# Kernel optimization log

Measured on AMD Instinct MI355X. Metric: run time of the kernel, lower is better.

## Reference

```python
import jax, jax.numpy as jnp
import numpy as np

MESSAGE_SIZE = 128
MESSAGE_PASSES = 3
N_BONDS = 7      # Single, Double, Triple, Quadruple, Aromatic, Pi, Universal
N_LAYERS = 8     # 8 bias-free Linear layers, ReLU after the first 7
N_TYPES = 6      # top-4 ranked atoms + atom 0, plus catchall slot (index 5)
ATOM_VALS = [6.0, 7.0, 8.0, 9.0, 16.0, 17.0, 1.0]
TOP_ATOMS = [6.0, 7.0, 8.0, 9.0, 0.0]


def setup_inputs() -> dict:
    key = jax.random.key(0)
    ks = jax.random.split(key, 8)
    B, N, F, D = 128, 128, 75, MESSAGE_SIZE
    g = jax.random.uniform(ks[0], (B, N_BONDS, N, N), dtype=jnp.float32)
    h = jax.random.normal(ks[1], (B, N, F), dtype=jnp.float32)
    # channel 0 carries the atomic number used for GRU routing
    atom_ids = jax.random.randint(ks[2], (B, N), 0, len(ATOM_VALS))
    h = h.at[:, :, 0].set(jnp.asarray(ATOM_VALS, jnp.float32)[atom_ids])
    s = 1.0 / np.sqrt(D)
    msg_W = jax.random.normal(ks[3], (N_BONDS, N_LAYERS, D, D), jnp.float32) * s
    gru_Wih = jax.random.normal(ks[4], (2, N_TYPES, 3 * D, D), jnp.float32) * s  # [regular/universal, type, 3H, H]
    gru_Whh = jax.random.normal(ks[5], (2, N_TYPES, 3 * D, D), jnp.float32) * s
    gru_bih = jax.random.normal(ks[6], (2, N_TYPES, 3 * D), jnp.float32) * s
    gru_bhh = jax.random.normal(ks[7], (2, N_TYPES, 3 * D), jnp.float32) * s
    return dict(g=g, h=h, msg_W=msg_W, gru_Wih=gru_Wih, gru_Whh=gru_Whh,
                gru_bih=gru_bih, gru_bhh=gru_bhh)


def _gru_grouped(x, hx, tid, Wih, Whh, bih, bhh):
    """torch.nn.GRUCell(input=x, hx=hx) with per-node parameter group tid in [0,T).
    Wih/Whh: [T, 3H, H], bih/bhh: [T, 3H]."""
    gx = jnp.einsum('nd,tgd->ntg', x, Wih)   # [n, T, 3H]
    gh = jnp.einsum('nd,tgd->ntg', hx, Whh)
    gx = jnp.take_along_axis(gx, tid[:, None, None], axis=1)[:, 0] + bih[tid]
    gh = jnp.take_along_axis(gh, tid[:, None, None], axis=1)[:, 0] + bhh[tid]
    xr, xz, xn = jnp.split(gx, 3, axis=-1)
    hr, hz, hn = jnp.split(gh, 3, axis=-1)
    r = jax.nn.sigmoid(xr + hr)
    z = jax.nn.sigmoid(xz + hz)
    n = jnp.tanh(xn + r * hn)
    return (1.0 - z) * n + z * hx


def reference(g, h, msg_W, gru_Wih, gru_Whh, gru_bih, gru_bhh):
    B, N, F = h.shape
    D = msg_W.shape[-1]
    h_t = jnp.concatenate([h, jnp.zeros((B, N, D - F), h.dtype)], axis=2)  # [B,N,D]
    atoms = h[:, :, 0].reshape(-1)
    tid = jnp.full(atoms.shape, N_TYPES - 1, jnp.int32)  # default catchall
    for i, a in enumerate(TOP_ATOMS):
        tid = jnp.where(atoms == jnp.float32(a), jnp.int32(i), tid)
    for _ in range(MESSAGE_PASSES):
        # per-bond-type 8-layer bias-free MLP, vectorized over the 7 bond types
        xb = jnp.broadcast_to(h_t[None], (N_BONDS, B, N, D))
        for l in range(N_LAYERS):
            xb = jnp.einsum('kbnd,ked->kbne', xb, msg_W[:, l])
            if l < N_LAYERS - 1:
                xb = jax.nn.relu(xb)
        # bmm aggregation per bond type: m_k = g[:,k] @ xb_k
        m_all = jnp.einsum('bknm,kbmd->kbnd', g, xb)
        m_non = m_all[:N_BONDS - 1].sum(0).reshape(-1, D)
        m_uni = m_all[N_BONDS - 1].reshape(-1, D)
        h_flat = h_t.reshape(-1, D)
        out = _gru_grouped(h_flat, m_non, tid, gru_Wih[0], gru_Whh[0], gru_bih[0], gru_bhh[0])
        out_u = _gru_grouped(h_flat, m_uni, tid, gru_Wih[1], gru_Whh[1], gru_bih[1], gru_bhh[1])
        h_t = (out + out_u).reshape(B, N, D)
    return h_t
```

## Files before the change

kernel.cpp:

```cpp
#include <hip/hip_runtime.h>
#include <math.h>

#define NBOND 7
#define NLAY 8
#define NTYPE 6
#define NNODES 16384
#define PX 136
#define NDESC 264

typedef _Float16 half8 __attribute__((ext_vector_type(8)));
typedef _Float16 half4 __attribute__((ext_vector_type(4)));
typedef float floatx16 __attribute__((ext_vector_type(16)));

__device__ __forceinline__ float sig_(float x) { return 1.0f / (1.0f + __expf(-x)); }
__device__ __forceinline__ int drow_(int reg, int hi) { return (reg & 3) + 8 * (reg >> 2) + 4 * hi; }

__device__ __forceinline__ _Float16 hi_(float v) { return (_Float16)v; }
__device__ __forceinline__ _Float16 lo_(float v) { return (_Float16)(v - (float)(_Float16)v); }

__global__ void setup_kernel(const float* __restrict__ h, float* __restrict__ hT,
                             int* __restrict__ counts, int* __restrict__ bucket)
{
    int gid = blockIdx.x * 256 + threadIdx.x;
    int node = gid >> 7, d = gid & 127;
    hT[gid] = (d < 75) ? h[node * 75 + d] : 0.0f;
    if (gid < NNODES) {
        float a = h[gid * 75];
        int tt = 5;
        if      (a == 6.0f) tt = 0;
        else if (a == 7.0f) tt = 1;
        else if (a == 8.0f) tt = 2;
        else if (a == 9.0f) tt = 3;
        else if (a == 0.0f) tt = 4;
        int slot = atomicAdd(&counts[tt], 1);
        bucket[tt * NNODES + slot] = gid;
    }
}

__global__ void build_desc_kernel(const int* __restrict__ counts, int* __restrict__ desc)
{
    if (threadIdx.x != 0 || blockIdx.x != 0) return;
    int i = 0;
    for (int tt = 0; tt < NTYPE; ++tt) {
        int nb = (counts[tt] + 63) >> 6;
        for (int s = 0; s < nb; ++s) desc[i++] = tt | (s << 3);
    }
    while (i < NDESC) desc[i++] = -1;
}

__global__ void pack_msg_kernel(const float* __restrict__ msgW, _Float16* __restrict__ Wp)
{
    int idx = blockIdx.x * 256 + threadIdx.x;
    if (idx >= NBOND * NLAY * 16 * 128) return;
    int e  = idx & 127;
    int c  = (idx >> 7) & 15;
    int kl = idx >> 11;
    const float* src = msgW + ((size_t)kl * 128 + e) * 128 + c * 8;
    float4 u = *(const float4*)src;
    float4 v = *(const float4*)(src + 4);
    float av[8] = {u.x, u.y, u.z, u.w, v.x, v.y, v.z, v.w};
    half8 hh, ll;
    #pragma unroll
    for (int j = 0; j < 8; ++j) { hh[j] = hi_(av[j]); ll[j] = lo_(av[j]); }
    _Float16* dst = Wp + ((size_t)kl * 16 + c) * 2048;
    *(half8*)(dst + e * 8)        = hh;
    *(half8*)(dst + 1024 + e * 8) = ll;
}

__global__ void pack_gru_kernel(const float* __restrict__ Wih, const float* __restrict__ Whh,
                                _Float16* __restrict__ Wp)
{
    int idx = blockIdx.x * 256 + threadIdx.x;
    if (idx >= 2 * NTYPE * 2 * 16 * 384) return;
    int col = idx % 384;
    int c   = (idx / 384) & 15;
    int vm  = idx / 6144;
    int mat = vm & 1;
    int vt  = vm >> 1;
    const float* src = (mat ? Whh : Wih) + ((size_t)vt * 384 + col) * 128 + c * 8;
    float4 u = *(const float4*)src;
    float4 v = *(const float4*)(src + 4);
    float av[8] = {u.x, u.y, u.z, u.w, v.x, v.y, v.z, v.w};
    half8 hh, ll;
    #pragma unroll
    for (int j = 0; j < 8; ++j) { hh[j] = hi_(av[j]); ll[j] = lo_(av[j]); }
    _Float16* dst = Wp + (size_t)vm * 98304 + (size_t)c * 6144;
    *(half8*)(dst + col * 8)        = hh;
    *(half8*)(dst + 3072 + col * 8) = ll;
}

__global__ __launch_bounds__(512, 4) void mlp_agg_mfma(
    const float* __restrict__ hin, const _Float16* __restrict__ Wp,
    const float* __restrict__ gmat, float* __restrict__ m_non, float* __restrict__ m_uni)
{
    __shared__ _Float16 Xhi[128 * PX];
    __shared__ _Float16 Xlo[128 * PX];

    const int bid = blockIdx.x;
    const int w12 = (bid & 7) * 112 + (bid >> 3);
    const int kb = w12 >> 7, b = w12 & 127;
    const int t = threadIdx.x;
    const int wave = t >> 6, lane = t & 63, lo = lane & 31, hi = lane >> 5;
    const int ctw = wave & 3, rh = wave >> 2;
    const int wcol = ctw * 32 + lo;

    for (int q = t; q < 128 * 32; q += 512) {
        int r = q >> 5, c4 = q & 31;
        float4 v = *(const float4*)(hin + ((size_t)(b * 128 + r)) * 128 + c4 * 4);
        half4 hh, ll;
        hh[0] = hi_(v.x); ll[0] = lo_(v.x);
        hh[1] = hi_(v.y); ll[1] = lo_(v.y);
        hh[2] = hi_(v.z); ll[2] = lo_(v.z);
        hh[3] = hi_(v.w); ll[3] = lo_(v.w);
        *(half4*)(Xhi + r * PX + c4 * 4) = hh;
        *(half4*)(Xlo + r * PX + c4 * 4) = ll;
    }
    __syncthreads();

    floatx16 acc[2];

    #pragma unroll 1
    for (int l = 0; l < NLAY; ++l) {
        #pragma unroll
        for (int r2 = 0; r2 < 2; ++r2) acc[r2] = (floatx16)0.0f;
        const _Float16* wb = Wp + ((size_t)(kb * NLAY + l) * 16) * 2048;

        #pragma unroll
        for (int kk = 0; kk < 8; ++kk) {
            const _Float16* bp = wb + (size_t)(kk * 2 + hi) * 2048;
            half8 b_h = *(const half8*)(bp + wcol * 8);
            half8 b_l = *(const half8*)(bp + 1024 + wcol * 8);
            #pragma unroll
            for (int r2 = 0; r2 < 2; ++r2) {
                int rrow = (rh * 2 + r2) * 32 + lo;
                half8 a_h = *(const half8*)(Xhi + rrow * PX + kk * 16 + hi * 8);
                half8 a_l = *(const half8*)(Xlo + rrow * PX + kk * 16 + hi * 8);
                acc[r2] = __builtin_amdgcn_mfma_f32_32x32x16_f16(a_h, b_h, acc[r2], 0, 0, 0);
                acc[r2] = __builtin_amdgcn_mfma_f32_32x32x16_f16(a_h, b_l, acc[r2], 0, 0, 0);
                acc[r2] = __builtin_amdgcn_mfma_f32_32x32x16_f16(a_l, b_h, acc[r2], 0, 0, 0);
            }
        }
        __syncthreads();

        if (l < NLAY - 1) {
            #pragma unroll
            for (int r2 = 0; r2 < 2; ++r2)
                #pragma unroll
                for (int reg = 0; reg < 16; ++reg) {
                    int n = (rh * 2 + r2) * 32 + drow_(reg, hi);
                    float vv = fmaxf(acc[r2][reg], 0.0f);
                    Xhi[n * PX + wcol] = hi_(vv);
                    Xlo[n * PX + wcol] = lo_(vv);
                }
        } else {
            #pragma unroll
            for (int r2 = 0; r2 < 2; ++r2)
                #pragma unroll
                for (int s = 0; s < 4; ++s) {
                    int m0 = (rh * 2 + r2) * 32 + 8 * s + 4 * hi;
                    half4 hh, ll;
                    #pragma unroll
                    for (int j = 0; j < 4; ++j) {
                        float vv = acc[r2][4 * s + j];
                        hh[j] = hi_(vv); ll[j] = lo_(vv);
                    }
                    *(half4*)(Xhi + wcol * PX + m0) = hh;
                    *(half4*)(Xlo + wcol * PX + m0) = ll;
                }
        }
        __syncthreads();
    }

    const int rtw = wave & 3, ch = wave >> 2;
    const int row = rtw * 32 + lo;
    #pragma unroll
    for (int c2 = 0; c2 < 2; ++c2) acc[c2] = (floatx16)0.0f;
    const float* grow = gmat + (size_t)(b * NBOND + kb) * 16384;

    #pragma unroll 2
    for (int kk = 0; kk < 8; ++kk) {
        const float* gp = grow + (size_t)row * 128 + kk * 16 + hi * 8;
        float4 u = *(const float4*)gp, v2 = *(const float4*)(gp + 4);
        float av[8] = {u.x, u.y, u.z, u.w, v2.x, v2.y, v2.z, v2.w};
        half8 a_h, a_l;
        #pragma unroll
        for (int j = 0; j < 8; ++j) { a_h[j] = hi_(av[j]); a_l[j] = lo_(av[j]); }
        #pragma unroll
        for (int c2 = 0; c2 < 2; ++c2) {
            int ct = ch * 2 + c2;
            half8 b_h = *(const half8*)(Xhi + (ct * 32 + lo) * PX + kk * 16 + hi * 8);
            half8 b_l = *(const half8*)(Xlo + (ct * 32 + lo) * PX + kk * 16 + hi * 8);
            acc[c2] = __builtin_amdgcn_mfma_f32_32x32x16_f16(a_h, b_h, acc[c2], 0, 0, 0);
            acc[c2] = __builtin_amdgcn_mfma_f32_32x32x16_f16(a_h, b_l, acc[c2], 0, 0, 0);
            acc[c2] = __builtin_amdgcn_mfma_f32_32x32x16_f16(a_l, b_h, acc[c2], 0, 0, 0);
        }
    }

    if (kb == NBOND - 1) {
        #pragma unroll
        for (int c2 = 0; c2 < 2; ++c2)
            #pragma unroll
            for (int reg = 0; reg < 16; ++reg) {
                int n = rtw * 32 + drow_(reg, hi);
                m_uni[((size_t)(b * 128 + n)) * 128 + (ch * 2 + c2) * 32 + lo] = acc[c2][reg];
            }
    } else {
        #pragma unroll
        for (int c2 = 0; c2 < 2; ++c2)
            #pragma unroll
            for (int reg = 0; reg < 16; ++reg) {
                int n = rtw * 32 + drow_(reg, hi);
                atomicAdd(m_non + ((size_t)(b * 128 + n)) * 128 + (ch * 2 + c2) * 32 + lo,
                          acc[c2][reg]);
            }
    }
}

__global__ __launch_bounds__(256, 2) void gru_mfma(
    float* __restrict__ hT,
    const float* __restrict__ m_non, const float* __restrict__ m_uni,
    const int* __restrict__ counts, const int* __restrict__ bucket,
    const int* __restrict__ desc,
    const _Float16* __restrict__ Wp, const float* __restrict__ bihp, const float* __restrict__ bhhp)
{
    __shared__ _Float16 Xh[64 * PX], Xl[64 * PX], Mh[64 * PX], Ml[64 * PX];
    __shared__ int bl[64];

    const int bid = blockIdx.x;
    const int dv = desc[(bid & 7) * (NDESC / 8) + (bid >> 3)];
    if (dv < 0) return;
    const int tt = dv & 7;
    const int base = (dv >> 3) * 64;
    const int t = threadIdx.x;
    const int cnt = counts[tt];
    const int nn = min(64, cnt - base);
    if (t < 64) bl[t] = (t < nn) ? bucket[tt * NNODES + base + t] : -1;
    __syncthreads();

    for (int q = t; q < 64 * 32; q += 256) {
        int r = q >> 5, c4 = q & 31;
        float4 xv = make_float4(0.f, 0.f, 0.f, 0.f);
        int node = bl[r];
        if (node >= 0) xv = *(const float4*)(hT + (size_t)node * 128 + c4 * 4);
        half4 hh, ll;
        hh[0] = hi_(xv.x); ll[0] = lo_(xv.x);
        hh[1] = hi_(xv.y); ll[1] = lo_(xv.y);
        hh[2] = hi_(xv.z); ll[2] = lo_(xv.z);
        hh[3] = hi_(xv.w); ll[3] = lo_(xv.w);
        *(half4*)(Xh + r * PX + c4 * 4) = hh;
        *(half4*)(Xl + r * PX + c4 * 4) = ll;
    }

    const int wave = t >> 6, lane = t & 63, lo = lane & 31, hi = lane >> 5;
    const int d = wave * 32 + lo;

    #pragma unroll 1
    for (int v = 0; v < 2; ++v) {
        const float* msrc = v ? m_uni : m_non;
        __syncthreads();
        for (int q = t; q < 64 * 32; q += 256) {
            int r = q >> 5, c4 = q & 31;
            float4 mv = make_float4(0.f, 0.f, 0.f, 0.f);
            int node = bl[r];
            if (node >= 0) mv = *(const float4*)(msrc + (size_t)node * 128 + c4 * 4);
            half4 hh, ll;
            hh[0] = hi_(mv.x); ll[0] = lo_(mv.x);
            hh[1] = hi_(mv.y); ll[1] = lo_(mv.y);
            hh[2] = hi_(mv.z); ll[2] = lo_(mv.z);
            hh[3] = hi_(mv.w); ll[3] = lo_(mv.w);
            *(half4*)(Mh + r * PX + c4 * 4) = hh;
            *(half4*)(Ml + r * PX + c4 * 4) = ll;
        }
        __syncthreads();

        const int vt = v * NTYPE + tt;
        const _Float16* pih = Wp + (size_t)(vt * 2 + 0) * 98304;
        const _Float16* phh = Wp + (size_t)(vt * 2 + 1) * 98304;

        floatx16 ar[2], az[2], ax[2], ah[2];
        #pragma unroll
        for (int r2 = 0; r2 < 2; ++r2) {
            ar[r2] = (floatx16)0.0f; az[r2] = (floatx16)0.0f;
            ax[r2] = (floatx16)0.0f; ah[r2] = (floatx16)0.0f;
        }

        #pragma unroll 2
        for (int kk = 0; kk < 8; ++kk) {
            int koff = kk * 16 + hi * 8;
            half8 xh[2], xl[2], mh[2], ml[2];
            #pragma unroll
            for (int r2 = 0; r2 < 2; ++r2) {
                int rr = r2 * 32 + lo;
                xh[r2] = *(const half8*)(Xh + rr * PX + koff);
                xl[r2] = *(const half8*)(Xl + rr * PX + koff);
                mh[r2] = *(const half8*)(Mh + rr * PX + koff);
                ml[r2] = *(const half8*)(Ml + rr * PX + koff);
            }
            const _Float16* ci = pih + (size_t)(kk * 2 + hi) * 6144;
            const _Float16* ch = phh + (size_t)(kk * 2 + hi) * 6144;

            {
                half8 wh = *(const half8*)(ci + (0 + d) * 8);
                half8 wl = *(const half8*)(ci + 3072 + (0 + d) * 8);
                #pragma unroll
                for (int r2 = 0; r2 < 2; ++r2) {
                    ar[r2] = __builtin_amdgcn_mfma_f32_32x32x16_f16(xh[r2], wh, ar[r2], 0, 0, 0);
                    ar[r2] = __builtin_amdgcn_mfma_f32_32x32x16_f16(xh[r2], wl, ar[r2], 0, 0, 0);
                    ar[r2] = __builtin_amdgcn_mfma_f32_32x32x16_f16(xl[r2], wh, ar[r2], 0, 0, 0);
                }
            }
            {
                half8 wh = *(const half8*)(ch + (0 + d) * 8);
                half8 wl = *(const half8*)(ch + 3072 + (0 + d) * 8);
                #pragma unroll
                for (int r2 = 0; r2 < 2; ++r2) {
                    ar[r2] = __builtin_amdgcn_mfma_f32_32x32x16_f16(mh[r2], wh, ar[r2], 0, 0, 0);
                    ar[r2] = __builtin_amdgcn_mfma_f32_32x32x16_f16(mh[r2], wl, ar[r2], 0, 0, 0);
                    ar[r2] = __builtin_amdgcn_mfma_f32_32x32x16_f16(ml[r2], wh, ar[r2], 0, 0, 0);
                }
            }
            {
                half8 wh = *(const half8*)(ci + (128 + d) * 8);
                half8 wl = *(const half8*)(ci + 3072 + (128 + d) * 8);
                #pragma unroll
                for (int r2 = 0; r2 < 2; ++r2) {
                    az[r2] = __builtin_amdgcn_mfma_f32_32x32x16_f16(xh[r2], wh, az[r2], 0, 0, 0);
                    az[r2] = __builtin_amdgcn_mfma_f32_32x32x16_f16(xh[r2], wl, az[r2], 0, 0, 0);
                    az[r2] = __builtin_amdgcn_mfma_f32_32x32x16_f16(xl[r2], wh, az[r2], 0, 0, 0);
                }
            }
            {
                half8 wh = *(const half8*)(ch + (128 + d) * 8);
                half8 wl = *(const half8*)(ch + 3072 + (128 + d) * 8);
                #pragma unroll
                for (int r2 = 0; r2 < 2; ++r2) {
                    az[r2] = __builtin_amdgcn_mfma_f32_32x32x16_f16(mh[r2], wh, az[r2], 0, 0, 0);
                    az[r2] = __builtin_amdgcn_mfma_f32_32x32x16_f16(mh[r2], wl, az[r2], 0, 0, 0);
                    az[r2] = __builtin_amdgcn_mfma_f32_32x32x16_f16(ml[r2], wh, az[r2], 0, 0, 0);
                }
            }
            {
                half8 wh = *(const half8*)(ci + (256 + d) * 8);
                half8 wl = *(const half8*)(ci + 3072 + (256 + d) * 8);
                #pragma unroll
                for (int r2 = 0; r2 < 2; ++r2) {
                    ax[r2] = __builtin_amdgcn_mfma_f32_32x32x16_f16(xh[r2], wh, ax[r2], 0, 0, 0);
                    ax[r2] = __builtin_amdgcn_mfma_f32_32x32x16_f16(xh[r2], wl, ax[r2], 0, 0, 0);
                    ax[r2] = __builtin_amdgcn_mfma_f32_32x32x16_f16(xl[r2], wh, ax[r2], 0, 0, 0);
                }
            }
            {
                half8 wh = *(const half8*)(ch + (256 + d) * 8);
                half8 wl = *(const half8*)(ch + 3072 + (256 + d) * 8);
                #pragma unroll
                for (int r2 = 0; r2 < 2; ++r2) {
                    ah[r2] = __builtin_amdgcn_mfma_f32_32x32x16_f16(mh[r2], wh, ah[r2], 0, 0, 0);
                    ah[r2] = __builtin_amdgcn_mfma_f32_32x32x16_f16(mh[r2], wl, ah[r2], 0, 0, 0);
                    ah[r2] = __builtin_amdgcn_mfma_f32_32x32x16_f16(ml[r2], wh, ah[r2], 0, 0, 0);
                }
            }
        }

        const float* bi = bihp + (size_t)vt * 384;
        const float* bh = bhhp + (size_t)vt * 384;
        float b_r  = bi[d] + bh[d];
        float b_z  = bi[128 + d] + bh[128 + d];
        float b_in = bi[256 + d];
        float b_hn = bh[256 + d];
        #pragma unroll
        for (int r2 = 0; r2 < 2; ++r2)
            #pragma unroll
            for (int reg = 0; reg < 16; ++reg) {
                int n = r2 * 32 + drow_(reg, hi);
                int node = bl[n];
                if (node < 0) continue;
                float r  = sig_(ar[r2][reg] + b_r);
                float z  = sig_(az[r2][reg] + b_z);
                float nv = tanhf(ax[r2][reg] + b_in + r * (ah[r2][reg] + b_hn));
                float mv = msrc[(size_t)node * 128 + d];
                float val = (1.0f - z) * nv + z * mv;
                if (v == 0) hT[(size_t)node * 128 + d] = val;
                else        hT[(size_t)node * 128 + d] += val;
            }
    }
}

extern "C" void kernel_launch(void* const* d_in, const int* in_sizes, int n_in,
                              void* d_out, int out_size, void* d_ws, size_t ws_size,
                              hipStream_t stream) {
    const float* g    = (const float*)d_in[0];
    const float* h    = (const float*)d_in[1];
    const float* msgW = (const float*)d_in[2];
    const float* Wih  = (const float*)d_in[3];
    const float* Whh  = (const float*)d_in[4];
    const float* bih  = (const float*)d_in[5];
    const float* bhh  = (const float*)d_in[6];
    float* hT = (float*)d_out;

    char* ws = (char*)d_ws;
    float* m_non = (float*)ws;
    float* m_uni = m_non + (size_t)NNODES * 128;
    int* counts  = (int*)(ws + 2 * (size_t)NNODES * 128 * 4);
    int* bucket  = counts + 8;
    int* desc    = bucket + NTYPE * NNODES;
    _Float16* WpM = (_Float16*)(desc + NDESC);
    _Float16* WpG = WpM + (size_t)NBOND * NLAY * 16 * 2048;

    (void)hipMemsetAsync(counts, 0, 8 * sizeof(int), stream);
    setup_kernel<<<NNODES * 128 / 256, 256, 0, stream>>>(h, hT, counts, bucket);
    build_desc_kernel<<<1, 64, 0, stream>>>(counts, desc);
    pack_msg_kernel<<<(NBOND * NLAY * 16 * 128 + 255) / 256, 256, 0, stream>>>(msgW, WpM);
    pack_gru_kernel<<<(2 * NTYPE * 2 * 16 * 384 + 255) / 256, 256, 0, stream>>>(Wih, Whh, WpG);

    for (int pass = 0; pass < 3; ++pass) {
        (void)hipMemsetAsync(m_non, 0, (size_t)NNODES * 128 * 4, stream);
        mlp_agg_mfma<<<dim3(NBOND * 128), 512, 0, stream>>>(hT, WpM, g, m_non, m_uni);
        gru_mfma<<<dim3(NDESC), 256, 0, stream>>>(hT, m_non, m_uni, counts, bucket, desc,
                                                  WpG, bih, bhh);
    }
}
```

Baseline: 822.9 us.

## Split GRU regular/universal halves across grid y with ping-pong hidden buffers

The GRU kernel now launches a second grid dimension so the regular and universal GRU halves run in separate blocks. Each block accumulates its result into the output buffer with atomicAdd. Hidden state ping-pongs between a workspace buffer and the output, which adds a memset per pass. The MLP block-to-(bond,batch) mapping is also changed so each XCD slot handles a contiguous group of batches across all bond types. The intent is to double GRU parallelism and improve L2 locality of hidden-state reads, at the cost of an extra memset and float atomics on the output.

```diff
diff --git a/kernel.cpp b/kernel.cpp
--- a/kernel.cpp
+++ b/kernel.cpp
@@ -97,8 +97,8 @@
     __shared__ _Float16 Xlo[128 * PX];
 
     const int bid = blockIdx.x;
-    const int w12 = (bid & 7) * 112 + (bid >> 3);
-    const int kb = w12 >> 7, b = w12 & 127;
+    const int k8 = bid & 7, j = bid >> 3;
+    const int kb = j >> 4, b = k8 * 16 + (j & 15);
     const int t = threadIdx.x;
     const int wave = t >> 6, lane = t & 63, lo = lane & 31, hi = lane >> 5;
     const int ctw = wave & 3, rh = wave >> 2;
@@ -160,9 +160,9 @@
                     int m0 = (rh * 2 + r2) * 32 + 8 * s + 4 * hi;
                     half4 hh, ll;
                     #pragma unroll
-                    for (int j = 0; j < 4; ++j) {
-                        float vv = acc[r2][4 * s + j];
-                        hh[j] = hi_(vv); ll[j] = lo_(vv);
+                    for (int j2 = 0; j2 < 4; ++j2) {
+                        float vv = acc[r2][4 * s + j2];
+                        hh[j2] = hi_(vv); ll[j2] = lo_(vv);
                     }
                     *(half4*)(Xhi + wcol * PX + m0) = hh;
                     *(half4*)(Xlo + wcol * PX + m0) = ll;
@@ -184,7 +184,7 @@
         float av[8] = {u.x, u.y, u.z, u.w, v2.x, v2.y, v2.z, v2.w};
         half8 a_h, a_l;
         #pragma unroll
-        for (int j = 0; j < 8; ++j) { a_h[j] = hi_(av[j]); a_l[j] = lo_(av[j]); }
+        for (int j2 = 0; j2 < 8; ++j2) { a_h[j2] = hi_(av[j2]); a_l[j2] = lo_(av[j2]); }
         #pragma unroll
         for (int c2 = 0; c2 < 2; ++c2) {
             int ct = ch * 2 + c2;
@@ -217,7 +217,7 @@
 }
 
 __global__ __launch_bounds__(256, 2) void gru_mfma(
-    float* __restrict__ hT,
+    const float* __restrict__ hin, float* __restrict__ hout,
     const float* __restrict__ m_non, const float* __restrict__ m_uni,
     const int* __restrict__ counts, const int* __restrict__ bucket,
     const int* __restrict__ desc,
@@ -230,6 +230,7 @@
     const int dv = desc[(bid & 7) * (NDESC / 8) + (bid >> 3)];
     if (dv < 0) return;
     const int tt = dv & 7;
+    const int v = blockIdx.y;
     const int base = (dv >> 3) * 64;
     const int t = threadIdx.x;
     const int cnt = counts[tt];
@@ -237,11 +238,17 @@
     if (t < 64) bl[t] = (t < nn) ? bucket[tt * NNODES + base + t] : -1;
     __syncthreads();
 
+    const float* msrc = v ? m_uni : m_non;
+
     for (int q = t; q < 64 * 32; q += 256) {
         int r = q >> 5, c4 = q & 31;
         float4 xv = make_float4(0.f, 0.f, 0.f, 0.f);
+        float4 mv = make_float4(0.f, 0.f, 0.f, 0.f);
         int node = bl[r];
-        if (node >= 0) xv = *(const float4*)(hT + (size_t)node * 128 + c4 * 4);
+        if (node >= 0) {
+            xv = *(const float4*)(hin  + (size_t)node * 128 + c4 * 4);
+            mv = *(const float4*)(msrc + (size_t)node * 128 + c4 * 4);
+        }
         half4 hh, ll;
         hh[0] = hi_(xv.x); ll[0] = lo_(xv.x);
         hh[1] = hi_(xv.y); ll[1] = lo_(xv.y);
@@ -249,140 +256,124 @@
         hh[3] = hi_(xv.w); ll[3] = lo_(xv.w);
         *(half4*)(Xh + r * PX + c4 * 4) = hh;
         *(half4*)(Xl + r * PX + c4 * 4) = ll;
-    }
+        hh[0] = hi_(mv.x); ll[0] = lo_(mv.x);
+        hh[1] = hi_(mv.y); ll[1] = lo_(mv.y);
+        hh[2] = hi_(mv.z); ll[2] = lo_(mv.z);
+        hh[3] = hi_(mv.w); ll[3] = lo_(mv.w);
+        *(half4*)(Mh + r * PX + c4 * 4) = hh;
+        *(half4*)(Ml + r * PX + c4 * 4) = ll;
+    }
+    __syncthreads();
 
     const int wave = t >> 6, lane = t & 63, lo = lane & 31, hi = lane >> 5;
     const int d = wave * 32 + lo;
-
-    #pragma unroll 1
-    for (int v = 0; v < 2; ++v) {
-        const float* msrc = v ? m_uni : m_non;
-        __syncthreads();
-        for (int q = t; q < 64 * 32; q += 256) {
-            int r = q >> 5, c4 = q & 31;
-            float4 mv = make_float4(0.f, 0.f, 0.f, 0.f);
-            int node = bl[r];
-            if (node >= 0) mv = *(const float4*)(msrc + (size_t)node * 128 + c4 * 4);
-            half4 hh, ll;
-            hh[0] = hi_(mv.x); ll[0] = lo_(mv.x);
-            hh[1] = hi_(mv.y); ll[1] = lo_(mv.y);
-            hh[2] = hi_(mv.z); ll[2] = lo_(mv.z);
-            hh[3] = hi_(mv.w); ll[3] = lo_(mv.w);
-            *(half4*)(Mh + r * PX + c4 * 4) = hh;
-            *(half4*)(Ml + r * PX + c4 * 4) = ll;
-        }
-        __syncthreads();
-
-        const int vt = v * NTYPE + tt;
-        const _Float16* pih = Wp + (size_t)(vt * 2 + 0) * 98304;
-        const _Float16* phh = Wp + (size_t)(vt * 2 + 1) * 98304;
-
-        floatx16 ar[2], az[2], ax[2], ah[2];
+    const int vt = v * NTYPE + tt;
+    const _Float16* pih = Wp + (size_t)(vt * 2 + 0) * 98304;
+    const _Float16* phh = Wp + (size_t)(vt * 2 + 1) * 98304;
+
+    floatx16 ar[2], az[2], ax[2], ah[2];
+    #pragma unroll
+    for (int r2 = 0; r2 < 2; ++r2) {
+        ar[r2] = (floatx16)0.0f; az[r2] = (floatx16)0.0f;
+        ax[r2] = (floatx16)0.0f; ah[r2] = (floatx16)0.0f;
+    }
+
+    #pragma unroll 2
+    for (int kk = 0; kk < 8; ++kk) {
+        int koff = kk * 16 + hi * 8;
+        half8 xh[2], xl[2], mh[2], ml[2];
         #pragma unroll
         for (int r2 = 0; r2 < 2; ++r2) {
-            ar[r2] = (floatx16)0.0f; az[r2] = (floatx16)0.0f;
-            ax[r2] = (floatx16)0.0f; ah[r2] = (floatx16)0.0f;
-        }
-
-        #pragma unroll 2
-        for (int kk = 0; kk < 8; ++kk) {
-            int koff = kk * 16 + hi * 8;
-            half8 xh[2], xl[2], mh[2], ml[2];
-            #pragma unroll
-            for (int r2 = 0; r2 < 2; ++r2) {
-                int rr = r2 * 32 + lo;
-                xh[r2] = *(const half8*)(Xh + rr * PX + koff);
-                xl[r2] = *(const half8*)(Xl + rr * PX + koff);
-                mh[r2] = *(const half8*)(Mh + rr * PX + koff);
-                ml[r2] = *(const half8*)(Ml + rr * PX + koff);
-            }
-            const _Float16* ci = pih + (size_t)(kk * 2 + hi) * 6144;
-            const _Float16* ch = phh + (size_t)(kk * 2 + hi) * 6144;
-
-            {
-                half8 wh = *(const half8*)(ci + (0 + d) * 8);
-                half8 wl = *(const half8*)(ci + 3072 + (0 + d) * 8);
-                #pragma unroll
-                for (int r2 = 0; r2 < 2; ++r2) {
-                    ar[r2] = __builtin_amdgcn_mfma_f32_32x32x16_f16(xh[r2], wh, ar[r2], 0, 0, 0);
-                    ar[r2] = __builtin_amdgcn_mfma_f32_32x32x16_f16(xh[r2], wl, ar[r2], 0, 0, 0);
-                    ar[r2] = __builtin_amdgcn_mfma_f32_32x32x16_f16(xl[r2], wh, ar[r2], 0, 0, 0);
-                }
-            }
-            {
-                half8 wh = *(const half8*)(ch + (0 + d) * 8);
-                half8 wl = *(const half8*)(ch + 3072 + (0 + d) * 8);
-                #pragma unroll
-                for (int r2 = 0; r2 < 2; ++r2) {
-                    ar[r2] = __builtin_amdgcn_mfma_f32_32x32x16_f16(mh[r2], wh, ar[r2], 0, 0, 0);
-                    ar[r2] = __builtin_amdgcn_mfma_f32_32x32x16_f16(mh[r2], wl, ar[r2], 0, 0, 0);
-                    ar[r2] = __builtin_amdgcn_mfma_f32_32x32x16_f16(ml[r2], wh, ar[r2], 0, 0, 0);
-                }
-            }
-            {
-                half8 wh = *(const half8*)(ci + (128 + d) * 8);
-                half8 wl = *(const half8*)(ci + 3072 + (128 + d) * 8);
-                #pragma unroll
-                for (int r2 = 0; r2 < 2; ++r2) {
-                    az[r2] = __builtin_amdgcn_mfma_f32_32x32x16_f16(xh[r2], wh, az[r2], 0, 0, 0);
-                    az[r2] = __builtin_amdgcn_mfma_f32_32x32x16_f16(xh[r2], wl, az[r2], 0, 0, 0);
-                    az[r2] = __builtin_amdgcn_mfma_f32_32x32x16_f16(xl[r2], wh, az[r2], 0, 0, 0);
-                }
-            }
-            {
-                half8 wh = *(const half8*)(ch + (128 + d) * 8);
-                half8 wl = *(const half8*)(ch + 3072 + (128 + d) * 8);
-                #pragma unroll
-                for (int r2 = 0; r2 < 2; ++r2) {
-                    az[r2] = __builtin_amdgcn_mfma_f32_32x32x16_f16(mh[r2], wh, az[r2], 0, 0, 0);
-                    az[r2] = __builtin_amdgcn_mfma_f32_32x32x16_f16(mh[r2], wl, az[r2], 0, 0, 0);
-                    az[r2] = __builtin_amdgcn_mfma_f32_32x32x16_f16(ml[r2], wh, az[r2], 0, 0, 0);
-                }
-            }
-            {
-                half8 wh = *(const half8*)(ci + (256 + d) * 8);
-                half8 wl = *(const half8*)(ci + 3072 + (256 + d) * 8);
-                #pragma unroll
-                for (int r2 = 0; r2 < 2; ++r2) {
-                    ax[r2] = __builtin_amdgcn_mfma_f32_32x32x16_f16(xh[r2], wh, ax[r2], 0, 0, 0);
-                    ax[r2] = __builtin_amdgcn_mfma_f32_32x32x16_f16(xh[r2], wl, ax[r2], 0, 0, 0);
-                    ax[r2] = __builtin_amdgcn_mfma_f32_32x32x16_f16(xl[r2], wh, ax[r2], 0, 0, 0);
-                }
-            }
-            {
-                half8 wh = *(const half8*)(ch + (256 + d) * 8);
-                half8 wl = *(const half8*)(ch + 3072 + (256 + d) * 8);
-                #pragma unroll
-                for (int r2 = 0; r2 < 2; ++r2) {
-                    ah[r2] = __builtin_amdgcn_mfma_f32_32x32x16_f16(mh[r2], wh, ah[r2], 0, 0, 0);
-                    ah[r2] = __builtin_amdgcn_mfma_f32_32x32x16_f16(mh[r2], wl, ah[r2], 0, 0, 0);
-                    ah[r2] = __builtin_amdgcn_mfma_f32_32x32x16_f16(ml[r2], wh, ah[r2], 0, 0, 0);
-                }
-            }
-        }
-
-        const float* bi = bihp + (size_t)vt * 384;
-        const float* bh = bhhp + (size_t)vt * 384;
-        float b_r  = bi[d] + bh[d];
-        float b_z  = bi[128 + d] + bh[128 + d];
-        float b_in = bi[256 + d];
-        float b_hn = bh[256 + d];
-        #pragma unroll
-        for (int r2 = 0; r2 < 2; ++r2)
-            #pragma unroll
-            for (int reg = 0; reg < 16; ++reg) {
-                int n = r2 * 32 + drow_(reg, hi);
-                int node = bl[n];
-                if (node < 0) continue;
-                float r  = sig_(ar[r2][reg] + b_r);
-                float z  = sig_(az[r2][reg] + b_z);
-                float nv = tanhf(ax[r2][reg] + b_in + r * (ah[r2][reg] + b_hn));
-                float mv = msrc[(size_t)node * 128 + d];
-                float val = (1.0f - z) * nv + z * mv;
-                if (v == 0) hT[(size_t)node * 128 + d] = val;
-                else        hT[(size_t)node * 128 + d] += val;
-            }
-    }
+            int rr = r2 * 32 + lo;
+            xh[r2] = *(const half8*)(Xh + rr * PX + koff);
+            xl[r2] = *(const half8*)(Xl + rr * PX + koff);
+            mh[r2] = *(const half8*)(Mh + rr * PX + koff);
+            ml[r2] = *(const half8*)(Ml + rr * PX + koff);
+        }
+        const _Float16* ci = pih + (size_t)(kk * 2 + hi) * 6144;
+        const _Float16* ch = phh + (size_t)(kk * 2 + hi) * 6144;
+
+        {
+            half8 wh = *(const half8*)(ci + (0 + d) * 8);
+            half8 wl = *(const half8*)(ci + 3072 + (0 + d) * 8);
+            #pragma unroll
+            for (int r2 = 0; r2 < 2; ++r2) {
+                ar[r2] = __builtin_amdgcn_mfma_f32_32x32x16_f16(xh[r2], wh, ar[r2], 0, 0, 0);
+                ar[r2] = __builtin_amdgcn_mfma_f32_32x32x16_f16(xh[r2], wl, ar[r2], 0, 0, 0);
+                ar[r2] = __builtin_amdgcn_mfma_f32_32x32x16_f16(xl[r2], wh, ar[r2], 0, 0, 0);
+            }
+        }
+        {
+            half8 wh = *(const half8*)(ch + (0 + d) * 8);
+            half8 wl = *(const half8*)(ch + 3072 + (0 + d) * 8);
+            #pragma unroll
+            for (int r2 = 0; r2 < 2; ++r2) {
+                ar[r2] = __builtin_amdgcn_mfma_f32_32x32x16_f16(mh[r2], wh, ar[r2], 0, 0, 0);
+                ar[r2] = __builtin_amdgcn_mfma_f32_32x32x16_f16(mh[r2], wl, ar[r2], 0, 0, 0);
+                ar[r2] = __builtin_amdgcn_mfma_f32_32x32x16_f16(ml[r2], wh, ar[r2], 0, 0, 0);
+            }
+        }
+        {
+            half8 wh = *(const half8*)(ci + (128 + d) * 8);
+            half8 wl = *(const half8*)(ci + 3072 + (128 + d) * 8);
+            #pragma unroll
+            for (int r2 = 0; r2 < 2; ++r2) {
+                az[r2] = __builtin_amdgcn_mfma_f32_32x32x16_f16(xh[r2], wh, az[r2], 0, 0, 0);
+                az[r2] = __builtin_amdgcn_mfma_f32_32x32x16_f16(xh[r2], wl, az[r2], 0, 0, 0);
+                az[r2] = __builtin_amdgcn_mfma_f32_32x32x16_f16(xl[r2], wh, az[r2], 0, 0, 0);
+            }
+        }
+        {
+            half8 wh = *(const half8*)(ch + (128 + d) * 8);
+            half8 wl = *(const half8*)(ch + 3072 + (128 + d) * 8);
+            #pragma unroll
+            for (int r2 = 0; r2 < 2; ++r2) {
+                az[r2] = __builtin_amdgcn_mfma_f32_32x32x16_f16(mh[r2], wh, az[r2], 0, 0, 0);
+                az[r2] = __builtin_amdgcn_mfma_f32_32x32x16_f16(mh[r2], wl, az[r2], 0, 0, 0);
+                az[r2] = __builtin_amdgcn_mfma_f32_32x32x16_f16(ml[r2], wh, az[r2], 0, 0, 0);
+            }
+        }
+        {
+            half8 wh = *(const half8*)(ci + (256 + d) * 8);
+            half8 wl = *(const half8*)(ci + 3072 + (256 + d) * 8);
+            #pragma unroll
+            for (int r2 = 0; r2 < 2; ++r2) {
+                ax[r2] = __builtin_amdgcn_mfma_f32_32x32x16_f16(xh[r2], wh, ax[r2], 0, 0, 0);
+                ax[r2] = __builtin_amdgcn_mfma_f32_32x32x16_f16(xh[r2], wl, ax[r2], 0, 0, 0);
+                ax[r2] = __builtin_amdgcn_mfma_f32_32x32x16_f16(xl[r2], wh, ax[r2], 0, 0, 0);
+            }
+        }
+        {
+            half8 wh = *(const half8*)(ch + (256 + d) * 8);
+            half8 wl = *(const half8*)(ch + 3072 + (256 + d) * 8);
+            #pragma unroll
+            for (int r2 = 0; r2 < 2; ++r2) {
+                ah[r2] = __builtin_amdgcn_mfma_f32_32x32x16_f16(mh[r2], wh, ah[r2], 0, 0, 0);
+                ah[r2] = __builtin_amdgcn_mfma_f32_32x32x16_f16(mh[r2], wl, ah[r2], 0, 0, 0);
+                ah[r2] = __builtin_amdgcn_mfma_f32_32x32x16_f16(ml[r2], wh, ah[r2], 0, 0, 0);
+            }
+        }
+    }
+
+    const float* bi = bihp + (size_t)vt * 384;
+    const float* bh = bhhp + (size_t)vt * 384;
+    float b_r  = bi[d] + bh[d];
+    float b_z  = bi[128 + d] + bh[128 + d];
+    float b_in = bi[256 + d];
+    float b_hn = bh[256 + d];
+    #pragma unroll
+    for (int r2 = 0; r2 < 2; ++r2)
+        #pragma unroll
+        for (int reg = 0; reg < 16; ++reg) {
+            int n = r2 * 32 + drow_(reg, hi);
+            int node = bl[n];
+            if (node < 0) continue;
+            float r  = sig_(ar[r2][reg] + b_r);
+            float z  = sig_(az[r2][reg] + b_z);
+            float nv = tanhf(ax[r2][reg] + b_in + r * (ah[r2][reg] + b_hn));
+            float mv = msrc[(size_t)node * 128 + d];
+            atomicAdd(hout + (size_t)node * 128 + d, (1.0f - z) * nv + z * mv);
+        }
 }
 
 extern "C" void kernel_launch(void* const* d_in, const int* in_sizes, int n_in,
@@ -395,7 +386,7 @@
     const float* Whh  = (const float*)d_in[4];
     const float* bih  = (const float*)d_in[5];
     const float* bhh  = (const float*)d_in[6];
-    float* hT = (float*)d_out;
+    float* h1 = (float*)d_out;
 
     char* ws = (char*)d_ws;
     float* m_non = (float*)ws;
@@ -405,17 +396,21 @@
     int* desc    = bucket + NTYPE * NNODES;
     _Float16* WpM = (_Float16*)(desc + NDESC);
     _Float16* WpG = WpM + (size_t)NBOND * NLAY * 16 * 2048;
+    float* h0 = (float*)(WpG + (size_t)2 * NTYPE * 2 * 98304);
 
     (void)hipMemsetAsync(counts, 0, 8 * sizeof(int), stream);
-    setup_kernel<<<NNODES * 128 / 256, 256, 0, stream>>>(h, hT, counts, bucket);
+    setup_kernel<<<NNODES * 128 / 256, 256, 0, stream>>>(h, h0, counts, bucket);
     build_desc_kernel<<<1, 64, 0, stream>>>(counts, desc);
     pack_msg_kernel<<<(NBOND * NLAY * 16 * 128 + 255) / 256, 256, 0, stream>>>(msgW, WpM);
     pack_gru_kernel<<<(2 * NTYPE * 2 * 16 * 384 + 255) / 256, 256, 0, stream>>>(Wih, Whh, WpG);
 
+    const float* hin_p[3]  = {h0, h1, h0};
+    float*       hout_p[3] = {h1, h0, h1};
     for (int pass = 0; pass < 3; ++pass) {
         (void)hipMemsetAsync(m_non, 0, (size_t)NNODES * 128 * 4, stream);
-        mlp_agg_mfma<<<dim3(NBOND * 128), 512, 0, stream>>>(hT, WpM, g, m_non, m_uni);
-        gru_mfma<<<dim3(NDESC), 256, 0, stream>>>(hT, m_non, m_uni, counts, bucket, desc,
-                                                  WpG, bih, bhh);
-    }
-}
+        (void)hipMemsetAsync(hout_p[pass], 0, (size_t)NNODES * 128 * 4, stream);
+        mlp_agg_mfma<<<dim3(NBOND * 128), 512, 0, stream>>>(hin_p[pass], WpM, g, m_non, m_uni);
+        gru_mfma<<<dim3(NDESC, 2), 256, 0, stream>>>(hin_p[pass], hout_p[pass], m_non, m_uni,
+                                                     counts, bucket, desc, WpG, bih, bhh);
+    }
+}
```

After: 880.6 us. +7.0%, slower.
